# Performance work log

Hardware: AMD Instinct MI355X
Metric: run time of the kernel (lower is better)

## Reference

```python
import jax, jax.numpy as jnp
import numpy as np

B, T, F = 256, 2048, 2
H, O = 128, 2

def setup_inputs() -> dict:
    key = jax.random.key(0)
    ks = jax.random.split(key, 12)
    s_i = 1.0 / np.sqrt(F)
    s_h = 1.0 / np.sqrt(H)
    return {
        'x': jax.random.normal(ks[0], (B, T, F), jnp.float32),
        'h0': jnp.zeros((B, H), jnp.float32),
        # input-to-hidden kernels (flax GRUCell dense_i: no bias)
        'Wir': jax.random.uniform(ks[1], (F, H), jnp.float32, -s_i, s_i),
        'Wiz': jax.random.uniform(ks[2], (F, H), jnp.float32, -s_i, s_i),
        'Win': jax.random.uniform(ks[3], (F, H), jnp.float32, -s_i, s_i),
        # hidden-to-hidden kernels + biases (flax GRUCell dense_h: with bias)
        'Whr': jax.random.uniform(ks[4], (H, H), jnp.float32, -s_h, s_h),
        'Whz': jax.random.uniform(ks[5], (H, H), jnp.float32, -s_h, s_h),
        'Whn': jax.random.uniform(ks[6], (H, H), jnp.float32, -s_h, s_h),
        'bhr': jnp.zeros((H,), jnp.float32),
        'bhz': jnp.zeros((H,), jnp.float32),
        'bhn': jnp.zeros((H,), jnp.float32),
        # output Dense
        'Wd': jax.random.uniform(ks[7], (H, O), jnp.float32, -s_h, s_h),
        'bd': jnp.zeros((O,), jnp.float32),
    }

def reference(x, h0, Wir, Wiz, Win, Whr, Whz, Whn, bhr, bhz, bhn, Wd, bd):
    # Precompute input projections for all timesteps (same math, batched GEMM).
    xr = jnp.einsum('btf,fh->bth', x, Wir)  # [B,T,H]
    xz = jnp.einsum('btf,fh->bth', x, Wiz)
    xn = jnp.einsum('btf,fh->bth', x, Win)
    xs = jnp.stack([xr, xz, xn], axis=0).swapaxes(1, 2)  # [3,T,B,H]

    def step(h, gates):
        gr, gz, gn = gates  # each [B,H]
        r = jax.nn.sigmoid(gr + h @ Whr + bhr)
        z = jax.nn.sigmoid(gz + h @ Whz + bhz)
        n = jnp.tanh(gn + r * (h @ Whn + bhn))
        h_new = (1.0 - z) * n + z * h
        return h_new, h_new

    carry, ys = jax.lax.scan(step, h0, jnp.moveaxis(xs, 1, 0))  # ys: [T,B,H]
    ys = jnp.swapaxes(ys, 0, 1)  # [B,T,H]
    out = jnp.einsum('bth,ho->bto', ys, Wd) + bd
    return (carry, out)
```

## Files before the change

### kernel.cpp

```cpp
#include <hip/hip_runtime.h>
#include <math.h>

#define BB 256
#define TT 2048
#define FF 2
#define HH 128
#define OO 2
#define NT 256

typedef _Float16 h2 __attribute__((ext_vector_type(2)));

__device__ __forceinline__ float fast_rcp(float x) { return __builtin_amdgcn_rcpf(x); }
__device__ __forceinline__ float sigmoid_f(float x) { return fast_rcp(1.0f + __expf(-x)); }
__device__ __forceinline__ float tanh_f(float x) { return 1.0f - 2.0f * fast_rcp(1.0f + __expf(2.0f * x)); }

__device__ __forceinline__ float dot2(unsigned int hv, h2 w, float acc) {
#if __has_builtin(__builtin_amdgcn_fdot2)
    return __builtin_amdgcn_fdot2(__builtin_bit_cast(h2, hv), w, acc, false);
#else
    const h2 h = __builtin_bit_cast(h2, hv);
    acc = fmaf((float)h[0], (float)w[0], acc);
    return fmaf((float)h[1], (float)w[1], acc);
#endif
}

#define FOR32(M, P) \
  M(P,0)  M(P,1)  M(P,2)  M(P,3)  M(P,4)  M(P,5)  M(P,6)  M(P,7)  \
  M(P,8)  M(P,9)  M(P,10) M(P,11) M(P,12) M(P,13) M(P,14) M(P,15) \
  M(P,16) M(P,17) M(P,18) M(P,19) M(P,20) M(P,21) M(P,22) M(P,23) \
  M(P,24) M(P,25) M(P,26) M(P,27) M(P,28) M(P,29) M(P,30) M(P,31)

#define DECLW(P,i) h2 P##i;
#define LOADW(P,i) P##i[0] = (_Float16)Wcol[(kb + 2*(i)    ) * HH]; \
                   P##i[1] = (_Float16)Wcol[(kb + 2*(i) + 1) * HH];

#define DOTQ(P, Q, i0, i1, i2, i3, ACC)        \
    ACC = dot2(Q.x, P##i0, ACC);               \
    ACC = dot2(Q.y, P##i1, ACC);               \
    ACC = dot2(Q.z, P##i2, ACC);               \
    ACC = dot2(Q.w, P##i3, ACC);

__global__ __launch_bounds__(NT)
__attribute__((amdgpu_waves_per_eu(1, 1)))
void gru_persistent(const float* __restrict__ x, const float* __restrict__ h0,
                    const float* __restrict__ Wir, const float* __restrict__ Wiz,
                    const float* __restrict__ Win, const float* __restrict__ Whr,
                    const float* __restrict__ Whz, const float* __restrict__ Whn,
                    const float* __restrict__ bhr, const float* __restrict__ bhz,
                    const float* __restrict__ bhn, const float* __restrict__ Wd,
                    const float* __restrict__ bd, float* __restrict__ out)
{
    __shared__ float x_sh[TT * FF];
    __shared__ __align__(16) float    h32[2][HH];
    __shared__ __align__(16) _Float16 h16[2][HH];

    const int b    = blockIdx.x;
    const int tid  = threadIdx.x;
    const int j    = tid >> 1;
    const int ks   = tid & 1;
    const int kb   = ks * 64;
    const int wv   = tid >> 6;
    const int lane = tid & 63;
    const bool lead = (ks == 0);

    FOR32(DECLW, wr_) FOR32(DECLW, wz_) FOR32(DECLW, wn_)
    { const float* Wcol = Whr + j; FOR32(LOADW, wr_) }
    { const float* Wcol = Whz + j; FOR32(LOADW, wz_) }
    { const float* Wcol = Whn + j; FOR32(LOADW, wn_) }

    float br = 0.f, bz = 0.f, bn = 0.f;
    float wir0 = 0.f, wir1 = 0.f, wiz0 = 0.f, wiz1 = 0.f, win0 = 0.f, win1 = 0.f;
    if (lead) {
        br = bhr[j]; bz = bhz[j]; bn = bhn[j];
        wir0 = Wir[j]; wir1 = Wir[HH + j];
        wiz0 = Wiz[j]; wiz1 = Wiz[HH + j];
        win0 = Win[j]; win1 = Win[HH + j];
    }

    float wdA0 = 0.f, wdA1 = 0.f, wdB0 = 0.f, wdB1 = 0.f, bd0 = 0.f, bd1 = 0.f;
    if (wv == 0) {
        wdA0 = Wd[lane * OO + 0];        wdA1 = Wd[lane * OO + 1];
        wdB0 = Wd[(lane + 64) * OO + 0]; wdB1 = Wd[(lane + 64) * OO + 1];
        bd0 = bd[0]; bd1 = bd[1];
    }

    {
        const float4* xi = reinterpret_cast<const float4*>(x + (size_t)b * TT * FF);
        float4* xo = reinterpret_cast<float4*>(x_sh);
        #pragma unroll
        for (int i = 0; i < 4; ++i) xo[tid + i * NT] = xi[tid + i * NT];
    }
    if (tid < HH) {
        const float hv = h0[b * HH + tid];
        h32[0][tid] = hv;
        h16[0][tid] = (_Float16)hv;
    }
    __syncthreads();

    float* __restrict__ yout = out + BB * HH;

    for (int t = 0; t < TT; ++t) {
        const int bR = t & 1;
        const int bW = bR ^ 1;

        const uint4* hq = reinterpret_cast<const uint4*>(h16[bR]) + (ks << 3);
        const uint4 q0 = hq[0], q1 = hq[1], q2 = hq[2], q3 = hq[3];
        const uint4 q4 = hq[4], q5 = hq[5], q6 = hq[6], q7 = hq[7];

        float r0 = 0.f, r1 = 0.f, z0 = 0.f, z1 = 0.f, m0 = 0.f, m1 = 0.f;
        DOTQ(wr_, q0,  0,  1,  2,  3, r0) DOTQ(wr_, q1,  4,  5,  6,  7, r0)
        DOTQ(wr_, q2,  8,  9, 10, 11, r0) DOTQ(wr_, q3, 12, 13, 14, 15, r0)
        DOTQ(wr_, q4, 16, 17, 18, 19, r1) DOTQ(wr_, q5, 20, 21, 22, 23, r1)
        DOTQ(wr_, q6, 24, 25, 26, 27, r1) DOTQ(wr_, q7, 28, 29, 30, 31, r1)
        DOTQ(wz_, q0,  0,  1,  2,  3, z0) DOTQ(wz_, q1,  4,  5,  6,  7, z0)
        DOTQ(wz_, q2,  8,  9, 10, 11, z0) DOTQ(wz_, q3, 12, 13, 14, 15, z0)
        DOTQ(wz_, q4, 16, 17, 18, 19, z1) DOTQ(wz_, q5, 20, 21, 22, 23, z1)
        DOTQ(wz_, q6, 24, 25, 26, 27, z1) DOTQ(wz_, q7, 28, 29, 30, 31, z1)
        DOTQ(wn_, q0,  0,  1,  2,  3, m0) DOTQ(wn_, q1,  4,  5,  6,  7, m0)
        DOTQ(wn_, q2,  8,  9, 10, 11, m0) DOTQ(wn_, q3, 12, 13, 14, 15, m0)
        DOTQ(wn_, q4, 16, 17, 18, 19, m1) DOTQ(wn_, q5, 20, 21, 22, 23, m1)
        DOTQ(wn_, q6, 24, 25, 26, 27, m1) DOTQ(wn_, q7, 28, 29, 30, 31, m1)

        if (wv == 0 && t > 0) {
            const float hv0 = h32[bR][lane], hv1 = h32[bR][lane + 64];
            float p0 = hv0 * wdA0 + hv1 * wdB0;
            float p1 = hv0 * wdA1 + hv1 * wdB1;
            #pragma unroll
            for (int off = 32; off >= 1; off >>= 1) {
                p0 += __shfl_xor(p0, off);
                p1 += __shfl_xor(p1, off);
            }
            if (lane == 0)
                reinterpret_cast<float2*>(yout)[(size_t)b * TT + (t - 1)] =
                    make_float2(p0 + bd0, p1 + bd1);
        }

        float ra = r0 + r1, za = z0 + z1, ma = m0 + m1;
        ra += __shfl_xor(ra, 1);
        za += __shfl_xor(za, 1);
        ma += __shfl_xor(ma, 1);

        if (lead) {
            const float hold = h32[bR][j];
            const float x0 = x_sh[t * FF + 0];
            const float x1 = x_sh[t * FF + 1];
            const float r  = sigmoid_f(ra + br + x0 * wir0 + x1 * wir1);
            const float z  = sigmoid_f(za + bz + x0 * wiz0 + x1 * wiz1);
            const float n  = tanh_f(x0 * win0 + x1 * win1 + r * (ma + bn));
            const float hn = (1.0f - z) * n + z * hold;
            h32[bW][j] = hn;
            h16[bW][j] = (_Float16)hn;
        }

        __syncthreads();
    }

    if (wv == 0) {
        const float hv0 = h32[0][lane], hv1 = h32[0][lane + 64];
        float p0 = hv0 * wdA0 + hv1 * wdB0;
        float p1 = hv0 * wdA1 + hv1 * wdB1;
        #pragma unroll
        for (int off = 32; off >= 1; off >>= 1) {
            p0 += __shfl_xor(p0, off);
            p1 += __shfl_xor(p1, off);
        }
        if (lane == 0)
            reinterpret_cast<float2*>(yout)[(size_t)b * TT + (TT - 1)] =
                make_float2(p0 + bd0, p1 + bd1);
    }
    if (tid < HH) out[b * HH + tid] = h32[0][tid];
}

extern "C" void kernel_launch(void* const* d_in, const int* in_sizes, int n_in,
                              void* d_out, int out_size, void* d_ws, size_t ws_size,
                              hipStream_t stream) {
    const float* x   = (const float*)d_in[0];
    const float* h0  = (const float*)d_in[1];
    const float* Wir = (const float*)d_in[2];
    const float* Wiz = (const float*)d_in[3];
    const float* Win = (const float*)d_in[4];
    const float* Whr = (const float*)d_in[5];
    const float* Whz = (const float*)d_in[6];
    const float* Whn = (const float*)d_in[7];
    const float* bhr = (const float*)d_in[8];
    const float* bhz = (const float*)d_in[9];
    const float* bhn = (const float*)d_in[10];
    const float* Wd  = (const float*)d_in[11];
    const float* bd  = (const float*)d_in[12];
    float* out = (float*)d_out;

    gru_persistent<<<BB, NT, 0, stream>>>(x, h0, Wir, Wiz, Win, Whr, Whz, Whn,
                                          bhr, bhz, bhn, Wd, bd, out);
}
```

Measured before the change: 1.498 ms.

## Batch output projection over 64-step fp16 hidden-state history ring

Replaces the double-buffered fp32/fp16 hidden-state buffers with a 64-slot fp16 history ring in shared memory and keeps the fp32 previous state in a register of the owning thread. The per-step output Dense projection that ran on wave 0 inside the serial recurrence is removed. Every 64 steps all four waves compute the projection for the buffered rows in parallel, which adds one extra barrier per 64 steps. This shortens the critical per-step path, at the cost of computing outputs from fp16-rounded hidden states, which lowers output precision.

```diff
diff --git a/kernel.cpp b/kernel.cpp
--- a/kernel.cpp
+++ b/kernel.cpp
@@ -51,8 +51,7 @@
                     const float* __restrict__ bd, float* __restrict__ out)
 {
     __shared__ float x_sh[TT * FF];
-    __shared__ __align__(16) float    h32[2][HH];
-    __shared__ __align__(16) _Float16 h16[2][HH];
+    __shared__ __align__(16) _Float16 hist[64][HH];
 
     const int b    = blockIdx.x;
     const int tid  = threadIdx.x;
@@ -70,19 +69,20 @@
 
     float br = 0.f, bz = 0.f, bn = 0.f;
     float wir0 = 0.f, wir1 = 0.f, wiz0 = 0.f, wiz1 = 0.f, win0 = 0.f, win1 = 0.f;
+    float hold = 0.f;
     if (lead) {
         br = bhr[j]; bz = bhz[j]; bn = bhn[j];
         wir0 = Wir[j]; wir1 = Wir[HH + j];
         wiz0 = Wiz[j]; wiz1 = Wiz[HH + j];
         win0 = Win[j]; win1 = Win[HH + j];
+        hold = h0[b * HH + j];
     }
 
-    float wdA0 = 0.f, wdA1 = 0.f, wdB0 = 0.f, wdB1 = 0.f, bd0 = 0.f, bd1 = 0.f;
-    if (wv == 0) {
-        wdA0 = Wd[lane * OO + 0];        wdA1 = Wd[lane * OO + 1];
-        wdB0 = Wd[(lane + 64) * OO + 0]; wdB1 = Wd[(lane + 64) * OO + 1];
-        bd0 = bd[0]; bd1 = bd[1];
-    }
+    const float wdA0 = Wd[lane * OO + 0];
+    const float wdA1 = Wd[lane * OO + 1];
+    const float wdB0 = Wd[(lane + 64) * OO + 0];
+    const float wdB1 = Wd[(lane + 64) * OO + 1];
+    const float bd0 = bd[0], bd1 = bd[1];
 
     {
         const float4* xi = reinterpret_cast<const float4*>(x + (size_t)b * TT * FF);
@@ -90,20 +90,15 @@
         #pragma unroll
         for (int i = 0; i < 4; ++i) xo[tid + i * NT] = xi[tid + i * NT];
     }
-    if (tid < HH) {
-        const float hv = h0[b * HH + tid];
-        h32[0][tid] = hv;
-        h16[0][tid] = (_Float16)hv;
-    }
+    if (tid < HH) hist[63][tid] = (_Float16)h0[b * HH + tid];
     __syncthreads();
 
     float* __restrict__ yout = out + BB * HH;
 
     for (int t = 0; t < TT; ++t) {
-        const int bR = t & 1;
-        const int bW = bR ^ 1;
+        const int sR = (t + 63) & 63;
 
-        const uint4* hq = reinterpret_cast<const uint4*>(h16[bR]) + (ks << 3);
+        const uint4* hq = reinterpret_cast<const uint4*>(hist[sR]) + (ks << 3);
         const uint4 q0 = hq[0], q1 = hq[1], q2 = hq[2], q3 = hq[3];
         const uint4 q4 = hq[4], q5 = hq[5], q6 = hq[6], q7 = hq[7];
 
@@ -121,54 +116,48 @@
         DOTQ(wn_, q4, 16, 17, 18, 19, m1) DOTQ(wn_, q5, 20, 21, 22, 23, m1)
         DOTQ(wn_, q6, 24, 25, 26, 27, m1) DOTQ(wn_, q7, 28, 29, 30, 31, m1)
 
-        if (wv == 0 && t > 0) {
-            const float hv0 = h32[bR][lane], hv1 = h32[bR][lane + 64];
-            float p0 = hv0 * wdA0 + hv1 * wdB0;
-            float p1 = hv0 * wdA1 + hv1 * wdB1;
-            #pragma unroll
-            for (int off = 32; off >= 1; off >>= 1) {
-                p0 += __shfl_xor(p0, off);
-                p1 += __shfl_xor(p1, off);
-            }
-            if (lane == 0)
-                reinterpret_cast<float2*>(yout)[(size_t)b * TT + (t - 1)] =
-                    make_float2(p0 + bd0, p1 + bd1);
-        }
-
         float ra = r0 + r1, za = z0 + z1, ma = m0 + m1;
         ra += __shfl_xor(ra, 1);
         za += __shfl_xor(za, 1);
         ma += __shfl_xor(ma, 1);
 
         if (lead) {
-            const float hold = h32[bR][j];
             const float x0 = x_sh[t * FF + 0];
             const float x1 = x_sh[t * FF + 1];
             const float r  = sigmoid_f(ra + br + x0 * wir0 + x1 * wir1);
             const float z  = sigmoid_f(za + bz + x0 * wiz0 + x1 * wiz1);
             const float n  = tanh_f(x0 * win0 + x1 * win1 + r * (ma + bn));
             const float hn = (1.0f - z) * n + z * hold;
-            h32[bW][j] = hn;
-            h16[bW][j] = (_Float16)hn;
+            hold = hn;
+            hist[t & 63][j] = (_Float16)hn;
         }
 
         __syncthreads();
+
+        if ((t & 63) == 63) {
+            const int t0 = t - 63;
+            #pragma unroll 4
+            for (int i = 0; i < 16; ++i) {
+                const int row = t0 + (wv << 4) + i;
+                const int s   = row & 63;
+                const float hv0 = (float)hist[s][lane];
+                const float hv1 = (float)hist[s][lane + 64];
+                float p0 = hv0 * wdA0 + hv1 * wdB0;
+                float p1 = hv0 * wdA1 + hv1 * wdB1;
+                #pragma unroll
+                for (int off = 32; off >= 1; off >>= 1) {
+                    p0 += __shfl_xor(p0, off);
+                    p1 += __shfl_xor(p1, off);
+                }
+                if (lane == 0)
+                    reinterpret_cast<float2*>(yout)[(size_t)b * TT + row] =
+                        make_float2(p0 + bd0, p1 + bd1);
+            }
+            __syncthreads();
+        }
     }
 
-    if (wv == 0) {
-        const float hv0 = h32[0][lane], hv1 = h32[0][lane + 64];
-        float p0 = hv0 * wdA0 + hv1 * wdB0;
-        float p1 = hv0 * wdA1 + hv1 * wdB1;
-        #pragma unroll
-        for (int off = 32; off >= 1; off >>= 1) {
-            p0 += __shfl_xor(p0, off);
-            p1 += __shfl_xor(p1, off);
-        }
-        if (lane == 0)
-            reinterpret_cast<float2*>(yout)[(size_t)b * TT + (TT - 1)] =
-                make_float2(p0 + bd0, p1 + bd1);
-    }
-    if (tid < HH) out[b * HH + tid] = h32[0][tid];
+    if (lead) out[b * HH + j] = hold;
 }
 
 extern "C" void kernel_launch(void* const* d_in, const int* in_sizes, int n_in,
```

After: 1.203 ms. 19.7% less time.
